# Kernel tuning notes

Hardware: AMD Instinct MI355X
Metric: run time of the kernel (lower is better)

The kernel has to match this reference:

```python
import jax, jax.numpy as jnp
import numpy as np

T, B, C = 4, 2, 128
LT, LH, LW = 8, 32, 32
NUM_HEADS = 8
HEAD_DIM = C // NUM_HEADS
THETA = 0.7
V_TH = 1.0
TAU = 2.0  # spikingjelly LIFNode default tau
N_WIN = (2, 2, 2)
TOPK = 4
EPS = 1e-5
ATAN_ALPHA = 2.0  # spikingjelly surrogate.ATan default


@jax.custom_vjp
def spike(x):
    return (x >= 0.0).astype(x.dtype)

def _spike_fwd(x):
    return spike(x), x

def _spike_bwd(x, g):
    s = (jnp.pi / 2.0) * ATAN_ALPHA * x
    return (g * (ATAN_ALPHA / 2.0) / (1.0 + s * s),)

spike.defvjp(_spike_fwd, _spike_bwd)


def lif(x_seq):
    """Multi-step LIF: v'=v+(x-v)/tau, spike at v>=V_TH, hard reset to 0 (detached)."""
    def step(v, x):
        v = v + (x - v) / TAU
        s = spike(v - V_TH)
        v = v * (1.0 - jax.lax.stop_gradient(s))  # detach_reset, v_reset=0
        return v, s
    _, s_seq = jax.lax.scan(step, jnp.zeros_like(x_seq[0]), x_seq)
    return s_seq


def bn(x, gamma, beta):
    # BatchNorm3d(track_running_stats=False) on [T*B, C, D, H, W]: batch stats per channel
    mean = x.mean(axis=(0, 1, 3, 4, 5), keepdims=True)
    var = x.var(axis=(0, 1, 3, 4, 5), keepdims=True)
    shp = (1, 1, -1, 1, 1, 1)
    return (x - mean) * jax.lax.rsqrt(var + EPS) * gamma.reshape(shp) + beta.reshape(shp)


def conv3d(x, w, pad):
    t, b = x.shape[:2]
    y = jax.lax.conv_general_dilated(
        x.reshape((t * b,) + x.shape[2:]), w,
        window_strides=(1, 1, 1), padding=[(pad, pad)] * 3,
        dimension_numbers=('NCDHW', 'OIDHW', 'NCDHW'))
    return y.reshape((t, b) + y.shape[1:])


def cdc_t(x, w):
    out = conv3d(x, w, 1)
    # central-difference temporal term: 1x1x1 conv with summed first/last temporal slices
    kd = w[:, :, 0].sum((-1, -2)) + w[:, :, 2].sum((-1, -2))  # [O, I]
    return out - THETA * jnp.einsum('oi,tbidhw->tbodhw', kd, x)


def to_wins(t):
    wt, wh, ww = N_WIN
    Tn, Bn, Cn, Lt, Lh, Lw = t.shape
    lt, lh, lw = Lt // wt, Lh // wh, Lw // ww
    t = t.reshape(Tn, Bn, Cn, wt, lt, wh, lh, ww, lw)
    t = t.transpose(0, 1, 3, 5, 7, 4, 6, 8, 2)
    return t.reshape(Tn, Bn, wt * wh * ww, lt * lh * lw, Cn)


def setup_inputs() -> dict:
    key = jax.random.key(0)
    ks = jax.random.split(key, 4)
    x = jax.random.normal(ks[0], (T, B, C, LT, LH, LW), jnp.float32)
    qw = jax.random.normal(ks[1], (C, C, 3, 3, 3), jnp.float32) / np.sqrt(C * 27)
    kw = jax.random.normal(ks[2], (C, C), jnp.float32) / np.sqrt(C)
    pw = jax.random.normal(ks[3], (C, C), jnp.float32) / np.sqrt(C)
    ones = jnp.ones((C,), jnp.float32)
    zeros = jnp.zeros((C,), jnp.float32)
    return {"x": x, "qw": qw, "q_gamma": ones, "q_beta": zeros,
            "kw": kw, "k_gamma": ones, "k_beta": zeros,
            "v_gamma": ones, "v_beta": zeros,
            "pw": pw, "p_gamma": ones, "p_beta": zeros}


def reference(x, qw, q_gamma, q_beta, kw, k_gamma, k_beta,
              v_gamma, v_beta, pw, p_gamma, p_beta):
    Tn, Bn, Cn, Lt, Lh, Lw = x.shape
    wt, wh, ww = N_WIN
    num_wins = wt * wh * ww
    lt, lh, lw = Lt // wt, Lh // wh, Lw // ww

    q_real = bn(cdc_t(x, qw), q_gamma, q_beta)
    k_real = bn(jnp.einsum('oi,tbidhw->tbodhw', kw, x), k_gamma, k_beta)

    # region-level routing from pre-spike activations
    q_region = to_wins(q_real).mean(axis=(0, 3))  # [B, W, C]
    k_region = to_wins(k_real).mean(axis=(0, 3))
    a_r = jnp.einsum('bwc,bvc->bwv', q_region, k_region) * (HEAD_DIM ** -0.5)
    k_eff = min(TOPK, num_wins)
    _, idx = jax.lax.top_k(a_r, k_eff)  # [B, W, k]

    q = lif(q_real)
    k = lif(k_real)
    v = lif(bn(x, v_gamma, v_beta))
    q_w = to_wins(q)  # [T,B,W,S,C]
    k_w = to_wins(k)
    v_w = to_wins(v)

    # gather routed windows per (batch, target window), mean-aggregate over top-k
    gather = jax.vmap(lambda src_b, idx_b: src_b[:, idx_b], in_axes=(1, 0), out_axes=1)
    k_agg = gather(k_w, idx).mean(axis=3)  # [T,B,W,S,C]
    v_agg = gather(v_w, idx).mean(axis=3)

    S = q_w.shape[3]
    q_h = q_w.reshape(Tn, Bn, num_wins, S, NUM_HEADS, HEAD_DIM)
    k_h = k_agg.reshape(Tn, Bn, num_wins, S, NUM_HEADS, HEAD_DIM)
    v_h = v_agg.reshape(Tn, Bn, num_wins, S, NUM_HEADS, HEAD_DIM)

    attn = (q_h * k_h).sum(axis=5, keepdims=True)  # [T,B,W,S,H,1]
    attn = lif(attn)
    out = (attn * v_h).reshape(Tn, Bn, num_wins, S, Cn)

    out = out.reshape(Tn, Bn, wt, wh, ww, lt, lh, lw, Cn)
    out = out.transpose(0, 1, 8, 2, 5, 3, 6, 4, 7).reshape(Tn, Bn, Cn, Lt, Lh, Lw)

    out = lif(out)
    out = bn(jnp.einsum('oi,tbidhw->tbodhw', pw, out), p_gamma, p_beta)
    return out
```

## Files before the change

kernel.cpp:

```cpp
#include <hip/hip_runtime.h>

#define TT 4
#define BB 2
#define CC 128
#define DD 8
#define HHH 32
#define WWW 32
#define PP (DD*HHH*WWW)
#define TSTRIDE (BB*CC*PP)
#define NWIN 8
#define SSS 1024
#define NHEAD 8
#define HDIM 16
#define THETA 0.7f
#define VTH 1.0f
#define NPERC (TT*BB*PP)
#define EPSf 1e-5f

typedef unsigned short ushortT;
typedef unsigned char ucharT;
typedef _Float16 half_t;
typedef _Float16 f16x8 __attribute__((ext_vector_type(8)));
typedef float    f32x16 __attribute__((ext_vector_type(16)));

typedef const __attribute__((address_space(1))) void* as1_cvp;
typedef __attribute__((address_space(3))) void* as3_vp;

__global__ __launch_bounds__(256) void prep_wmodT(const float* __restrict__ qw,
                                                  float* __restrict__ wmodT) {
    int oi = blockIdx.x*256 + threadIdx.x;
    if (oi >= CC*CC) return;
    int o  = oi >> 7;
    int ic = oi & 127;
    const float* wp = qw + (size_t)oi*27;
    float kd = 0.f;
    #pragma unroll
    for (int t=0; t<9; t++) kd += wp[t] + wp[18+t];
    #pragma unroll
    for (int t=0; t<27; t++) {
        float v = wp[t] - ((t==13) ? THETA*kd : 0.f);
        wmodT[((size_t)o*27 + t)*CC + ic] = v;
    }
}

__global__ __launch_bounds__(256) void prep_wfrag(const float* __restrict__ wmodT,
                                                  half_t* __restrict__ wfrag) {
    int id = blockIdx.x*256 + threadIdx.x;
    if (id >= 8*27*4*64) return;
    int lane = id & 63;
    int r = id >> 6;
    int m = r & 3; r >>= 2;
    int t = r % 27;
    int kb = r / 27;
    int o   = m*32 + (lane & 31);
    int ic0 = kb*16 + (lane>>5)*8;
    size_t base = ((size_t)(id>>6))*2*64*8 + (size_t)lane*8;
    #pragma unroll
    for (int j=0;j<8;j++){
        float v = wmodT[((size_t)o*27 + t)*CC + ic0 + j];
        half_t h = (half_t)v;
        half_t l = (half_t)(v - (float)h);
        wfrag[base + 0*64*8 + j] = h;
        wfrag[base + 1*64*8 + j] = l;
    }
}

__global__ __launch_bounds__(256) void prep_w1frag(const float* __restrict__ W,
                                                   half_t* __restrict__ frag) {
    int id = blockIdx.x*256 + threadIdx.x;
    if (id >= 2048) return;
    int lane = id & 63;
    int r = id >> 6;
    int m = r & 3;
    int kb = r >> 2;
    int o   = m*32 + (lane & 31);
    int ic0 = kb*16 + (lane>>5)*8;
    size_t base = ((size_t)(kb*4+m))*2*64*8 + (size_t)lane*8;
    #pragma unroll
    for (int j=0;j<8;j++){
        float v = W[(size_t)o*CC + ic0 + j];
        half_t h = (half_t)v;
        half_t l = (half_t)(v - (float)h);
        frag[base + 0*64*8 + j] = h;
        frag[base + 1*64*8 + j] = l;
    }
}

__global__ __launch_bounds__(256) void build_xsplit(const float* __restrict__ x,
                                                    half_t* __restrict__ xsp) {
    int id = blockIdx.x*256 + threadIdx.x;
    if (id >= 8*16*8*34*34) return;
    int wt = id % 34; int r = id/34;
    int hp = r % 34;  r /= 34;
    int dz = r % 8;   r /= 8;
    int icg = r & 15; int tb = r >> 4;
    bool inb = (hp>=1) & (hp<=32) & (wt>=1) & (wt<=32);
    half_t h8[8], l8[8];
    #pragma unroll
    for (int j=0;j<8;j++){
        float v = 0.f;
        if (inb)
            v = x[((size_t)(tb*CC + icg*8+j))*PP + (size_t)dz*1024 + (hp-1)*32 + (wt-1)];
        half_t h = (half_t)v;
        half_t l = (half_t)(v - (float)h);
        h8[j]=h; l8[j]=l;
    }
    #pragma unroll
    for (int sp=0; sp<2; sp++){
        size_t gu = (((((size_t)tb*2 + sp)*16 + icg)*8 + dz)*34 + hp)*34 + wt;
        half_t* dst = xsp + gu*8;
        const half_t* src = (sp==0)?h8:l8;
        #pragma unroll
        for (int j=0;j<8;j++) dst[j] = src[j];
    }
}

__global__ __launch_bounds__(512,2) void conv_mfma3(const half_t* __restrict__ xsp,
                                                    const half_t* __restrict__ wfrag,
                                                    float* __restrict__ y0,
                                                    float* __restrict__ y1) {
    extern __shared__ half_t slab[];
    int tid  = threadIdx.x;
    int wid  = tid >> 6;
    int lane = tid & 63;
    int ln   = lane & 31;
    int half_ = lane >> 5;
    int hg = blockIdx.x;
    int dp = blockIdx.y;
    int z  = blockIdx.z;
    int tb = z >> 1, kh = z & 1;
    int H0 = hg*4, d0 = dp*4;
    int r  = wid & 3;
    int q  = wid >> 2;
    float* y = kh ? y1 : y0;

    auto STAGE = [&](int bk, int bsel) {
        int kb = kh*4 + bk;
        half_t* bufp = slab + (size_t)bsel*(4896*8);
        #pragma unroll 1
        for (int k2=0; k2<10; k2++) {
            int u = tid + (k2<<9);
            if (u < 4896) {
                int sp  = (u >= 2448) ? 1 : 0;
                int r1  = u - sp*2448;
                int icg = (r1 >= 1224) ? 1 : 0;
                int p2  = r1 - icg*1224;
                int dzs = p2/204; int r3 = p2 - dzs*204;
                int hp  = r3/34;  int wt = r3 - hp*34;
                int dd  = d0 - 1 + dzs;
                const half_t* src = ((unsigned)dd < 8u)
                    ? &xsp[((((((size_t)tb*2 + sp)*16 + (kb*2+icg))*8 + dd)*34 + (H0+hp))*34 + wt)*8]
                    : &xsp[(size_t)ln*8];
                __builtin_amdgcn_global_load_lds((as1_cvp)src,
                    (as3_vp)(bufp + (size_t)u*8), 16, 0, 0);
            }
        }
    };

    f32x16 acc[2][4];
    #pragma unroll
    for (int dt=0;dt<2;dt++)
        #pragma unroll
        for (int m=0;m<4;m++)
            #pragma unroll
            for (int i=0;i<16;i++) acc[dt][m][i] = 0.f;

    f16x8 ca[4][2];
    #pragma unroll
    for (int m=0;m<4;m++)
        #pragma unroll
        for (int sp=0;sp<2;sp++)
            ca[m][sp] = *(const f16x8*)&wfrag[((((size_t)(kh*4*27)*4 + m)*2+sp)*64 + lane)*8];

    asm volatile("" ::: "memory");
    STAGE(0,0);
    STAGE(1,1);
    asm volatile("" ::: "memory");

    #pragma unroll 1
    for (int kk=0; kk<4; kk++) {
        int kb = kh*4 + kk;
        if (kk == 0) {
            if (wid < 5) asm volatile("s_waitcnt vmcnt(10)" ::: "memory");
            else         asm volatile("s_waitcnt vmcnt(9)"  ::: "memory");
        } else {
            asm volatile("s_waitcnt vmcnt(63)" ::: "memory");
        }
        __builtin_amdgcn_s_barrier();
        asm volatile("" ::: "memory");
        const half_t* bufp = slab + (size_t)(kk&1)*(4896*8);
        #pragma unroll 1
        for (int t=0; t<27; t++) {
            int dz=t/9; int rr=t-dz*9; int dh=rr/3; int dw=rr-dh*3;
            f16x8 cb[2][2];
            #pragma unroll
            for (int dt=0;dt<2;dt++){
                int unitb = (q*2 + dt + dz)*204 + (r+dh)*34 + (ln+dw);
                #pragma unroll
                for (int sp=0;sp<2;sp++)
                    cb[dt][sp] = *(const f16x8*)&bufp[(size_t)((sp*2+half_)*1224 + unitb)*8];
            }
            f16x8 na[4][2];
            int nt  = (t<26)? t+1 : 0;
            int nkb = (t<26)? kb  : ((kk<3)? kb+1 : kb);
            #pragma unroll
            for (int m=0;m<4;m++)
                #pragma unroll
                for (int sp=0;sp<2;sp++)
                    na[m][sp] = *(const f16x8*)&wfrag[((((size_t)(nkb*27+nt)*4+m)*2+sp)*64 + lane)*8];
            __builtin_amdgcn_s_setprio(1);
            #pragma unroll
            for (int dt=0;dt<2;dt++)
                #pragma unroll
                for (int m=0;m<4;m++) acc[dt][m] = __builtin_amdgcn_mfma_f32_32x32x16_f16(ca[m][0], cb[dt][0], acc[dt][m],0,0,0);
            #pragma unroll
            for (int dt=0;dt<2;dt++)
                #pragma unroll
                for (int m=0;m<4;m++) acc[dt][m] = __builtin_amdgcn_mfma_f32_32x32x16_f16(ca[m][0], cb[dt][1], acc[dt][m],0,0,0);
            #pragma unroll
            for (int dt=0;dt<2;dt++)
                #pragma unroll
                for (int m=0;m<4;m++) acc[dt][m] = __builtin_amdgcn_mfma_f32_32x32x16_f16(ca[m][1], cb[dt][0], acc[dt][m],0,0,0);
            __builtin_amdgcn_s_setprio(0);
            #pragma unroll
            for (int m=0;m<4;m++)
                #pragma unroll
                for (int sp=0;sp<2;sp++) ca[m][sp] = na[m][sp];
        }
        asm volatile("" ::: "memory");
        __builtin_amdgcn_s_barrier();
        asm volatile("" ::: "memory");
        if (kk < 2) STAGE(kk+2, kk&1);
    }

    int h = H0 + r;
    #pragma unroll
    for (int dt=0; dt<2; dt++) {
        int d = d0 + q*2 + dt;
        #pragma unroll
        for (int m=0; m<4; m++) {
            #pragma unroll
            for (int reg=0; reg<16; reg++) {
                int row = (reg&3) + 8*(reg>>2) + 4*half_;
                int o = m*32 + row;
                y[((size_t)tb*CC + o)*PP + d*1024 + h*32 + ln] = acc[dt][m][reg];
            }
        }
    }
}

__global__ __launch_bounds__(256) void conv_add(float* __restrict__ q,
                                                const float* __restrict__ p1) {
    size_t i = ((size_t)blockIdx.x*256 + threadIdx.x)*4;
    float4 a = *(const float4*)&q[i];
    float4 b = *(const float4*)&p1[i];
    a.x+=b.x; a.y+=b.y; a.z+=b.z; a.w+=b.w;
    *(float4*)&q[i] = a;
}

__global__ __launch_bounds__(256) void kgemm_mfma(const half_t* __restrict__ xsp,
                                                  const half_t* __restrict__ wk,
                                                  float* __restrict__ y) {
    int tid  = threadIdx.x;
    int wid  = tid >> 6;
    int lane = tid & 63;
    int ln   = lane & 31;
    int half_ = lane >> 5;
    int hg = blockIdx.x, d = blockIdx.y, tb = blockIdx.z;
    int h = hg*4 + wid;

    f32x16 acc[4];
    #pragma unroll
    for (int m=0;m<4;m++)
        #pragma unroll
        for (int i=0;i<16;i++) acc[m][i] = 0.f;

    #pragma unroll 2
    for (int kb=0; kb<8; kb++) {
        f16x8 b[2];
        #pragma unroll
        for (int sp=0; sp<2; sp++) {
            size_t gu = (((((size_t)tb*2 + sp)*16 + (kb*2+half_))*8 + d)*34 + (h+1))*34 + (ln+1);
            b[sp] = *(const f16x8*)&xsp[gu*8];
        }
        #pragma unroll
        for (int m=0; m<4; m++) {
            const half_t* wb = wk + ((size_t)(kb*4+m))*2*64*8 + (size_t)lane*8;
            f16x8 a0 = *(const f16x8*)&wb[0*64*8];
            f16x8 a1 = *(const f16x8*)&wb[1*64*8];
            acc[m] = __builtin_amdgcn_mfma_f32_32x32x16_f16(a0, b[0], acc[m],0,0,0);
            acc[m] = __builtin_amdgcn_mfma_f32_32x32x16_f16(a0, b[1], acc[m],0,0,0);
            acc[m] = __builtin_amdgcn_mfma_f32_32x32x16_f16(a1, b[0], acc[m],0,0,0);
        }
    }
    #pragma unroll
    for (int m=0; m<4; m++) {
        #pragma unroll
        for (int reg=0; reg<16; reg++) {
            int row = (reg&3) + 8*(reg>>2) + 4*half_;
            int o = m*32 + row;
            y[((size_t)tb*CC + o)*PP + d*1024 + h*32 + ln] = acc[m][reg];
        }
    }
}

__global__ __launch_bounds__(256) void pgemm_mfma(const ushortT* __restrict__ spkb,
                                                  const half_t* __restrict__ wp,
                                                  float* __restrict__ y) {
    int tid  = threadIdx.x;
    int wid  = tid >> 6;
    int lane = tid & 63;
    int ln   = lane & 31;
    int half_ = lane >> 5;
    int hg = blockIdx.x, d = blockIdx.y, tb = blockIdx.z;
    int h = hg*4 + wid;
    int p = d*1024 + h*32 + ln;

    f32x16 acc[4];
    #pragma unroll
    for (int m=0;m<4;m++)
        #pragma unroll
        for (int i=0;i<16;i++) acc[m][i] = 0.f;

    #pragma unroll 2
    for (int kb=0; kb<8; kb++) {
        f16x8 b = *(const f16x8*)&spkb[(((size_t)tb*16 + (kb*2+half_))*PP + p)*8];
        #pragma unroll
        for (int m=0; m<4; m++) {
            const half_t* wb = wp + ((size_t)(kb*4+m))*2*64*8 + (size_t)lane*8;
            f16x8 a0 = *(const f16x8*)&wb[0*64*8];
            f16x8 a1 = *(const f16x8*)&wb[1*64*8];
            acc[m] = __builtin_amdgcn_mfma_f32_32x32x16_f16(a0, b, acc[m],0,0,0);
            acc[m] = __builtin_amdgcn_mfma_f32_32x32x16_f16(a1, b, acc[m],0,0,0);
        }
    }
    #pragma unroll
    for (int m=0; m<4; m++) {
        #pragma unroll
        for (int reg=0; reg<16; reg++) {
            int row = (reg&3) + 8*(reg>>2) + 4*half_;
            int o = m*32 + row;
            y[((size_t)tb*CC + o)*PP + p] = acc[m][reg];
        }
    }
}

__global__ __launch_bounds__(128) void win_stats(const float* __restrict__ q,
        const float* __restrict__ k, const float* __restrict__ x,
        float* __restrict__ rsum, float* __restrict__ rsq) {
    int blk = blockIdx.x;
    int src = blk >> 11;
    int r   = blk & 2047;
    const float* base = (src==0) ? q : ((src==1) ? k : x);
    int c  = r & 127;
    int wi = (r >> 7) & 7;
    int b  = r >> 10;
    int wd = wi>>2, wh = (wi>>1)&1, ww = wi&1;
    int tid = threadIdx.x;
    float s=0.f, s2=0.f;
    for (int t=0;t<TT;t++){
        const float* p = base + ((size_t)(t*BB+b)*CC + c)*PP;
        for (int si=tid; si<SSS; si+=128){
            int ld = si>>8, lh=(si>>4)&15, lw=si&15;
            float v = p[((wd*4+ld)<<10) + ((wh*16+lh)<<5) + (ww*16+lw)];
            s += v; s2 += v*v;
        }
    }
    __shared__ float ls[128], ls2[128];
    ls[tid]=s; ls2[tid]=s2; __syncthreads();
    for (int off=64;off>0;off>>=1){
        if(tid<off){ ls[tid]+=ls[tid+off]; ls2[tid]+=ls2[tid+off]; }
        __syncthreads();
    }
    if (tid==0){ rsum[blk]=ls[0]; rsq[blk]=ls2[0]; }
}

__global__ __launch_bounds__(384) void stats_fin(const float* __restrict__ rsum,
        const float* __restrict__ rsq, float* __restrict__ sums) {
    int tid = threadIdx.x;
    int src = tid >> 7, c = tid & 127;
    float s=0.f, s2=0.f;
    for (int bw=0; bw<16; bw++){
        int idx = src*2048 + bw*128 + c;
        s  += rsum[idx];
        s2 += rsq[idx];
    }
    sums[src*256 + c]       = s;
    sums[src*256 + 128 + c] = s2;
}

__global__ __launch_bounds__(128) void route_topk(const float* __restrict__ qreg,
        const float* __restrict__ kreg,
        const float* __restrict__ qsum, const float* __restrict__ qsq,
        const float* __restrict__ ksum, const float* __restrict__ ksq,
        const float* __restrict__ qg, const float* __restrict__ qb,
        const float* __restrict__ kg, const float* __restrict__ kb,
        int* __restrict__ idxout) {
    __shared__ float qn[16*128], kn[16*128], ar[16*8];
    int tid = threadIdx.x;
    for (int e=tid; e<16*128; e+=128){
        int c = e&127;
        float qm = qsum[c]*(1.f/NPERC);
        float qv = qsq[c]*(1.f/NPERC) - qm*qm;
        float qr = rsqrtf(qv + EPSf);
        qn[e] = (qreg[e]*(1.f/(TT*SSS)) - qm)*qr*qg[c] + qb[c];
        float km = ksum[c]*(1.f/NPERC);
        float kv = ksq[c]*(1.f/NPERC) - km*km;
        float kr = rsqrtf(kv + EPSf);
        kn[e] = (kreg[e]*(1.f/(TT*SSS)) - km)*kr*kg[c] + kb[c];
    }
    __syncthreads();
    {
        int b = tid>>6, w=(tid>>3)&7, v=tid&7;
        float s=0.f;
        for (int c=0;c<128;c++) s += qn[(b*8+w)*128+c]*kn[(b*8+v)*128+c];
        ar[(b*8+w)*8+v] = s * 0.25f;
    }
    __syncthreads();
    if (tid < 16){
        const float* row = &ar[tid*8];
        bool used[8] = {false,false,false,false,false,false,false,false};
        for (int j=0;j<4;j++){
            int best=0; float bv=-3.0e38f;
            for (int v=0; v<8; v++){
                if (!used[v] && row[v] > bv){ bv=row[v]; best=v; }
            }
            used[best]=true;
            idxout[tid*4+j]=best;
        }
    }
}

__global__ __launch_bounds__(256) void lif_bn_win3(const float* __restrict__ qin,
        const float* __restrict__ kin, const float* __restrict__ xin,
        ucharT* __restrict__ qs, ucharT* __restrict__ ks, ucharT* __restrict__ vs,
        const float* __restrict__ stats,
        const float* __restrict__ qg, const float* __restrict__ qb,
        const float* __restrict__ kg, const float* __restrict__ kb,
        const float* __restrict__ vg, const float* __restrict__ vb) {
    int src = blockIdx.y;
    const float* in  = (src==0) ? qin : ((src==1) ? kin : xin);
    ucharT*      spk = (src==0) ? qs  : ((src==1) ? ks  : vs);
    const float* gamma = (src==0) ? qg : ((src==1) ? kg : vg);
    const float* beta  = (src==0) ? qb : ((src==1) ? kb : vb);
    int e = blockIdx.x*256 + threadIdx.x;
    if (e >= BB*CC*PP) return;
    int p = e & (PP-1);
    int c = (e >> 13) & 127;
    int b = e >> 20;
    float mean = stats[src*256 + c]*(1.f/NPERC);
    float var  = stats[src*256 + 128 + c]*(1.f/NPERC) - mean*mean;
    float sc = rsqrtf(var+EPSf)*gamma[c];
    float sh = beta[c] - mean*sc;
    int d = p>>10, h=(p>>5)&31, w=p&31;
    int wi = ((d>>2)*2 + (h>>4))*2 + (w>>4);
    int si = (((d&3)<<4) + (h&15))*16 + (w&15);
    size_t widx = ((size_t)(b*NWIN+wi)*CC + c)*SSS + si;
    float v=0.f;
    #pragma unroll
    for (int t=0;t<TT;t++){
        float xn = in[(size_t)t*TSTRIDE + e]*sc + sh;
        v = (v+xn)*0.5f;
        float s = (v>=VTH)?1.f:0.f;
        spk[(size_t)t*TSTRIDE + widx] = (ucharT)(v>=VTH ? 1 : 0);
        v *= (1.f - s);
    }
}

__global__ __launch_bounds__(256) void attn_lif(const ucharT* __restrict__ qspk,
        const ucharT* __restrict__ kspk, const ucharT* __restrict__ vspk,
        const int* __restrict__ idx, ushortT* __restrict__ spkb) {
    int id = blockIdx.x*256 + threadIdx.x;
    if (id >= BB*NWIN*NHEAD*SSS) return;
    int s  = id & 1023;
    int hh = (id>>10) & 7;
    int wi = (id>>13) & 7;
    int b  = id>>16;
    int bw = b*NWIN+wi;
    size_t qbase = ((size_t)bw*CC + hh*HDIM)*SSS + s;
    size_t sbase[4];
    #pragma unroll
    for (int j=0;j<4;j++){
        int src = idx[bw*4+j];
        sbase[j] = ((size_t)(b*NWIN+src)*CC + hh*HDIM)*SSS + s;
    }
    int wd = wi>>2, wh = (wi>>1)&1, ww = wi&1;
    int d3 = wd*4 + (s>>8), h3 = wh*16 + ((s>>4)&15), w3 = ww*16 + (s&15);
    int p  = (d3<<10) + (h3<<5) + w3;

    float v=0.f;
    float v2[16];
    #pragma unroll
    for (int dd=0; dd<16; dd++) v2[dd]=0.f;

    #pragma unroll 1
    for (int t=0;t<TT;t++){
        size_t toff = (size_t)t*TSTRIDE;
        int km[16], vm[16];
        #pragma unroll
        for (int dd=0;dd<16;dd++){ km[dd]=0; vm[dd]=0; }
        #pragma unroll
        for (int j=0;j<4;j++){
            const ucharT* kp = kspk+toff+sbase[j];
            const ucharT* vp = vspk+toff+sbase[j];
            #pragma unroll
            for (int dd=0; dd<16; dd++){
                km[dd] += kp[(size_t)dd*SSS];
                vm[dd] += vp[(size_t)dd*SSS];
            }
        }
        const ucharT* qp = qspk+toff+qbase;
        int atti=0;
        #pragma unroll
        for (int dd=0;dd<16;dd++) atti += (int)qp[(size_t)dd*SSS]*km[dd];
        float att = (float)atti * 0.25f;
        v = (v+att)*0.5f;
        float sp = (v>=VTH)?1.f:0.f;
        v *= (1.f-sp);
        float spq = sp*0.25f;
        union { ushortT u[8]; uint4 q4; } pk0, pk1;
        #pragma unroll
        for (int dd=0;dd<16;dd++){
            float ov = spq*(float)vm[dd];
            v2[dd] = (v2[dd]+ov)*0.5f;
            float s2 = (v2[dd]>=VTH)?1.f:0.f;
            v2[dd] *= (1.f-s2);
            ushortT bs = (s2 != 0.f) ? (ushortT)0x3C00 : (ushortT)0;
            if (dd < 8) pk0.u[dd] = bs; else pk1.u[dd-8] = bs;
        }
        int tb2 = t*BB + b;
        size_t base = (((size_t)tb2*16 + hh*2)*PP + p)*8;
        *(uint4*)&spkb[base] = pk0.q4;
        *(uint4*)&spkb[base + (size_t)PP*8] = pk1.q4;
    }
}

__global__ __launch_bounds__(256) void pstats_part(const float* __restrict__ xin,
        float* __restrict__ part_sum, float* __restrict__ part_sq) {
    int blk = blockIdx.x;
    int c = blk & 127, tb = blk >> 7;
    int tid = threadIdx.x;
    const float* p = xin + ((size_t)tb*CC + c)*PP;
    float s=0.f, s2=0.f;
    for (int i=tid; i<PP; i+=256){ float v=p[i]; s+=v; s2+=v*v; }
    __shared__ float ls[256], ls2[256];
    ls[tid]=s; ls2[tid]=s2; __syncthreads();
    for (int off=128; off>0; off>>=1){
        if (tid<off){ ls[tid]+=ls[tid+off]; ls2[tid]+=ls2[tid+off]; }
        __syncthreads();
    }
    if (tid==0){ part_sum[blk]=ls[0]; part_sq[blk]=ls2[0]; }
}

__global__ __launch_bounds__(128) void pstats_fin(const float* __restrict__ part_sum,
        const float* __restrict__ part_sq, float* __restrict__ sum,
        float* __restrict__ sq) {
    int c = threadIdx.x;
    float s=0.f, s2=0.f;
    for (int tb=0; tb<8; tb++){
        s  += part_sum[tb*128+c];
        s2 += part_sq[tb*128+c];
    }
    sum[c]=s; sq[c]=s2;
}

__global__ __launch_bounds__(256) void bn_apply(const float* __restrict__ xin,
        float* __restrict__ yout,
        const float* __restrict__ sum, const float* __restrict__ sq,
        const float* __restrict__ gamma, const float* __restrict__ beta) {
    size_t i = (size_t)blockIdx.x*256 + threadIdx.x;
    if (i >= (size_t)TT*BB*CC*PP) return;
    int c = (int)((i>>13)&127);
    float mean = sum[c]*(1.f/NPERC);
    float var  = sq[c]*(1.f/NPERC) - mean*mean;
    float sc = rsqrtf(var+EPSf)*gamma[c];
    float sh = beta[c] - mean*sc;
    yout[i] = xin[i]*sc + sh;
}

extern "C" void kernel_launch(void* const* d_in, const int* in_sizes, int n_in,
                              void* d_out, int out_size, void* d_ws, size_t ws_size,
                              hipStream_t stream) {
    const float* x  = (const float*)d_in[0];
    const float* qw = (const float*)d_in[1];
    const float* qg = (const float*)d_in[2];
    const float* qb = (const float*)d_in[3];
    const float* kw = (const float*)d_in[4];
    const float* kg = (const float*)d_in[5];
    const float* kb = (const float*)d_in[6];
    const float* vg = (const float*)d_in[7];
    const float* vb = (const float*)d_in[8];
    const float* pw = (const float*)d_in[9];
    const float* pg = (const float*)d_in[10];
    const float* pb = (const float*)d_in[11];
    float* out = (float*)d_out;
    float* ws  = (float*)d_ws;

    const size_t NEL = (size_t)TT*TSTRIDE;
    float* qconv = ws;
    float* kconv = ws + NEL;
    float* qspk  = ws + 2*NEL;
    float* kspk  = ws + 3*NEL;
    float* vspk  = ws + 4*NEL;
    float* wmodT = ws + 5*NEL;
    float* stats = ws + 5*NEL + 442368;
    float *qsum=stats,     *qsq=stats+128,  *ksum=stats+256, *ksq=stats+384,
          *psum=stats+768, *psq=stats+896;
    float* rsum = stats + 1024;
    float* rsq  = rsum + 6144;
    float* ppart_sum = rsq + 6144;
    float* ppart_sq  = ppart_sum + 1024;
    int*   idxp = (int*)(ppart_sq + 1024);

    half_t* xsp    = (half_t*)(ws + 2*NEL);
    half_t* wfrag  = (half_t*)(ws + 4*NEL);
    half_t* wkfrag = (half_t*)(ws + 4*NEL) + 884736;
    half_t* wpfrag = (half_t*)(ws + 4*NEL);
    ushortT* spkb  = (ushortT*)(ws + NEL);
    float*   pconv = ws + 2*NEL;
    float*   part1 = kconv;

    prep_wmodT<<<64,256,0,stream>>>(qw, wmodT);
    prep_wfrag<<<216,256,0,stream>>>(wmodT, wfrag);
    prep_w1frag<<<8,256,0,stream>>>(kw, wkfrag);
    build_xsplit<<<4624,256,0,stream>>>(x, xsp);
    {
        static bool attr_set = false;
        const int shmem = 2*4896*8*(int)sizeof(half_t);
        if (!attr_set) {
            hipFuncSetAttribute((const void*)conv_mfma3,
                                hipFuncAttributeMaxDynamicSharedMemorySize, shmem);
            attr_set = true;
        }
        dim3 cg(8,2,16);
        conv_mfma3<<<cg,512,shmem,stream>>>(xsp, wfrag, qconv, part1);
    }
    conv_add<<<8192,256,0,stream>>>(qconv, part1);
    {
        dim3 gg(8,8,8);
        kgemm_mfma<<<gg,256,0,stream>>>(xsp, wkfrag, kconv);
    }
    win_stats<<<6144,128,0,stream>>>(qconv, kconv, x, rsum, rsq);
    stats_fin<<<1,384,0,stream>>>(rsum, rsq, stats);
    route_topk<<<1,128,0,stream>>>(rsum, rsum+2048, qsum,qsq,ksum,ksq,qg,qb,kg,kb,idxp);
    {
        dim3 lg(8192,3);
        lif_bn_win3<<<lg,256,0,stream>>>(qconv,kconv,x,
                                         (ucharT*)qspk,(ucharT*)kspk,(ucharT*)vspk,
                                         stats, qg,qb,kg,kb,vg,vb);
    }
    attn_lif<<<512,256,0,stream>>>((const ucharT*)qspk,(const ucharT*)kspk,
                                   (const ucharT*)vspk,idxp,spkb);
    prep_w1frag<<<8,256,0,stream>>>(pw, wpfrag);
    {
        dim3 gg(8,8,8);
        pgemm_mfma<<<gg,256,0,stream>>>(spkb, wpfrag, pconv);
    }
    pstats_part<<<1024,256,0,stream>>>(pconv, ppart_sum, ppart_sq);
    pstats_fin<<<1,128,0,stream>>>(ppart_sum, ppart_sq, psum, psq);
    bn_apply<<<32768,256,0,stream>>>(pconv, out, psum, psq, pg, pb);
}
```

Baseline: 419.7 us.

## Fuse conv partial-sum add into consumers and merge small reduction kernels

Drops the conv_add pass: the two conv partial outputs are summed on the fly inside win_stats and lif_bn_win3. stats_fin is merged into route_topk, and pstats_fin is folded into bn_apply, which now re-reduces the partials per thread. The workspace layout is reshuffled so both partial buffers stay live, and the setprio hints around the MFMA block are removed. This saves one full read-modify-write pass and two tiny launches, at the cost of an extra read wherever the q tensor is consumed and redundant partial-sum reads in bn_apply.

Result: faster. 396.8 us (-5.5%).

```diff
diff --git a/kernel.cpp b/kernel.cpp
--- a/kernel.cpp
+++ b/kernel.cpp
@@ -208,7 +208,6 @@
                 #pragma unroll
                 for (int sp=0;sp<2;sp++)
                     na[m][sp] = *(const f16x8*)&wfrag[((((size_t)(nkb*27+nt)*4+m)*2+sp)*64 + lane)*8];
-            __builtin_amdgcn_s_setprio(1);
             #pragma unroll
             for (int dt=0;dt<2;dt++)
                 #pragma unroll
@@ -221,7 +220,6 @@
             for (int dt=0;dt<2;dt++)
                 #pragma unroll
                 for (int m=0;m<4;m++) acc[dt][m] = __builtin_amdgcn_mfma_f32_32x32x16_f16(ca[m][1], cb[dt][0], acc[dt][m],0,0,0);
-            __builtin_amdgcn_s_setprio(0);
             #pragma unroll
             for (int m=0;m<4;m++)
                 #pragma unroll
@@ -247,15 +245,6 @@
             }
         }
     }
-}
-
-__global__ __launch_bounds__(256) void conv_add(float* __restrict__ q,
-                                                const float* __restrict__ p1) {
-    size_t i = ((size_t)blockIdx.x*256 + threadIdx.x)*4;
-    float4 a = *(const float4*)&q[i];
-    float4 b = *(const float4*)&p1[i];
-    a.x+=b.x; a.y+=b.y; a.z+=b.z; a.w+=b.w;
-    *(float4*)&q[i] = a;
 }
 
 __global__ __launch_bounds__(256) void kgemm_mfma(const half_t* __restrict__ xsp,
@@ -345,13 +334,14 @@
     }
 }
 
-__global__ __launch_bounds__(128) void win_stats(const float* __restrict__ q,
+__global__ __launch_bounds__(128) void win_stats(const float* __restrict__ q0,
+        const float* __restrict__ q1,
         const float* __restrict__ k, const float* __restrict__ x,
         float* __restrict__ rsum, float* __restrict__ rsq) {
     int blk = blockIdx.x;
     int src = blk >> 11;
     int r   = blk & 2047;
-    const float* base = (src==0) ? q : ((src==1) ? k : x);
+    const float* base = (src==0) ? q0 : ((src==1) ? k : x);
     int c  = r & 127;
     int wi = (r >> 7) & 7;
     int b  = r >> 10;
@@ -359,10 +349,14 @@
     int tid = threadIdx.x;
     float s=0.f, s2=0.f;
     for (int t=0;t<TT;t++){
-        const float* p = base + ((size_t)(t*BB+b)*CC + c)*PP;
+        size_t off0 = ((size_t)(t*BB+b)*CC + c)*PP;
+        const float* p  = base + off0;
+        const float* p2 = q1 + off0;
         for (int si=tid; si<SSS; si+=128){
             int ld = si>>8, lh=(si>>4)&15, lw=si&15;
-            float v = p[((wd*4+ld)<<10) + ((wh*16+lh)<<5) + (ww*16+lw)];
+            int o = ((wd*4+ld)<<10) + ((wh*16+lh)<<5) + (ww*16+lw);
+            float v = p[o];
+            if (src==0) v += p2[o];
             s += v; s2 += v*v;
         }
     }
@@ -375,42 +369,40 @@
     if (tid==0){ rsum[blk]=ls[0]; rsq[blk]=ls2[0]; }
 }
 
-__global__ __launch_bounds__(384) void stats_fin(const float* __restrict__ rsum,
-        const float* __restrict__ rsq, float* __restrict__ sums) {
-    int tid = threadIdx.x;
-    int src = tid >> 7, c = tid & 127;
-    float s=0.f, s2=0.f;
-    for (int bw=0; bw<16; bw++){
-        int idx = src*2048 + bw*128 + c;
-        s  += rsum[idx];
-        s2 += rsq[idx];
-    }
-    sums[src*256 + c]       = s;
-    sums[src*256 + 128 + c] = s2;
-}
-
-__global__ __launch_bounds__(128) void route_topk(const float* __restrict__ qreg,
-        const float* __restrict__ kreg,
-        const float* __restrict__ qsum, const float* __restrict__ qsq,
-        const float* __restrict__ ksum, const float* __restrict__ ksq,
+__global__ __launch_bounds__(384) void route_fin(const float* __restrict__ rsum,
+        const float* __restrict__ rsq,
         const float* __restrict__ qg, const float* __restrict__ qb,
         const float* __restrict__ kg, const float* __restrict__ kb,
-        int* __restrict__ idxout) {
+        float* __restrict__ stats, int* __restrict__ idxout) {
     __shared__ float qn[16*128], kn[16*128], ar[16*8];
+    __shared__ float csum[384], csq[384];
     int tid = threadIdx.x;
-    for (int e=tid; e<16*128; e+=128){
+    {
+        int src = tid >> 7, c = tid & 127;
+        float s=0.f, s2=0.f;
+        for (int bw=0; bw<16; bw++){
+            int idx = src*2048 + bw*128 + c;
+            s  += rsum[idx];
+            s2 += rsq[idx];
+        }
+        stats[src*256 + c]       = s;
+        stats[src*256 + 128 + c] = s2;
+        csum[tid]=s; csq[tid]=s2;
+    }
+    __syncthreads();
+    for (int e=tid; e<16*128; e+=384){
         int c = e&127;
-        float qm = qsum[c]*(1.f/NPERC);
-        float qv = qsq[c]*(1.f/NPERC) - qm*qm;
+        float qm = csum[c]*(1.f/NPERC);
+        float qv = csq[c]*(1.f/NPERC) - qm*qm;
         float qr = rsqrtf(qv + EPSf);
-        qn[e] = (qreg[e]*(1.f/(TT*SSS)) - qm)*qr*qg[c] + qb[c];
-        float km = ksum[c]*(1.f/NPERC);
-        float kv = ksq[c]*(1.f/NPERC) - km*km;
+        qn[e] = (rsum[e]*(1.f/(TT*SSS)) - qm)*qr*qg[c] + qb[c];
+        float km = csum[128+c]*(1.f/NPERC);
+        float kv = csq[128+c]*(1.f/NPERC) - km*km;
         float kr = rsqrtf(kv + EPSf);
-        kn[e] = (kreg[e]*(1.f/(TT*SSS)) - km)*kr*kg[c] + kb[c];
+        kn[e] = (rsum[2048+e]*(1.f/(TT*SSS)) - km)*kr*kg[c] + kb[c];
     }
     __syncthreads();
-    {
+    if (tid < 128){
         int b = tid>>6, w=(tid>>3)&7, v=tid&7;
         float s=0.f;
         for (int c=0;c<128;c++) s += qn[(b*8+w)*128+c]*kn[(b*8+v)*128+c];
@@ -431,7 +423,8 @@
     }
 }
 
-__global__ __launch_bounds__(256) void lif_bn_win3(const float* __restrict__ qin,
+__global__ __launch_bounds__(256) void lif_bn_win3(const float* __restrict__ q0,
+        const float* __restrict__ q1,
         const float* __restrict__ kin, const float* __restrict__ xin,
         ucharT* __restrict__ qs, ucharT* __restrict__ ks, ucharT* __restrict__ vs,
         const float* __restrict__ stats,
@@ -439,7 +432,7 @@
         const float* __restrict__ kg, const float* __restrict__ kb,
         const float* __restrict__ vg, const float* __restrict__ vb) {
     int src = blockIdx.y;
-    const float* in  = (src==0) ? qin : ((src==1) ? kin : xin);
+    const float* in  = (src==0) ? q0 : ((src==1) ? kin : xin);
     ucharT*      spk = (src==0) ? qs  : ((src==1) ? ks  : vs);
     const float* gamma = (src==0) ? qg : ((src==1) ? kg : vg);
     const float* beta  = (src==0) ? qb : ((src==1) ? kb : vb);
@@ -459,7 +452,10 @@
     float v=0.f;
     #pragma unroll
     for (int t=0;t<TT;t++){
-        float xn = in[(size_t)t*TSTRIDE + e]*sc + sh;
+        size_t ti = (size_t)t*TSTRIDE + e;
+        float raw = in[ti];
+        if (src==0) raw += q1[ti];
+        float xn = raw*sc + sh;
         v = (v+xn)*0.5f;
         float s = (v>=VTH)?1.f:0.f;
         spk[(size_t)t*TSTRIDE + widx] = (ucharT)(v>=VTH ? 1 : 0);
@@ -552,27 +548,21 @@
     if (tid==0){ part_sum[blk]=ls[0]; part_sq[blk]=ls2[0]; }
 }
 
-__global__ __launch_bounds__(128) void pstats_fin(const float* __restrict__ part_sum,
-        const float* __restrict__ part_sq, float* __restrict__ sum,
-        float* __restrict__ sq) {
-    int c = threadIdx.x;
-    float s=0.f, s2=0.f;
-    for (int tb=0; tb<8; tb++){
-        s  += part_sum[tb*128+c];
-        s2 += part_sq[tb*128+c];
-    }
-    sum[c]=s; sq[c]=s2;
-}
-
 __global__ __launch_bounds__(256) void bn_apply(const float* __restrict__ xin,
         float* __restrict__ yout,
-        const float* __restrict__ sum, const float* __restrict__ sq,
+        const float* __restrict__ part_sum, const float* __restrict__ part_sq,
         const float* __restrict__ gamma, const float* __restrict__ beta) {
     size_t i = (size_t)blockIdx.x*256 + threadIdx.x;
     if (i >= (size_t)TT*BB*CC*PP) return;
     int c = (int)((i>>13)&127);
-    float mean = sum[c]*(1.f/NPERC);
-    float var  = sq[c]*(1.f/NPERC) - mean*mean;
+    float s=0.f, s2=0.f;
+    #pragma unroll
+    for (int tb=0; tb<8; tb++){
+        s  += part_sum[tb*128+c];
+        s2 += part_sq[tb*128+c];
+    }
+    float mean = s*(1.f/NPERC);
+    float var  = s2*(1.f/NPERC) - mean*mean;
     float sc = rsqrtf(var+EPSf)*gamma[c];
     float sh = beta[c] - mean*sc;
     yout[i] = xin[i]*sc + sh;
@@ -597,28 +587,28 @@
     float* ws  = (float*)d_ws;
 
     const size_t NEL = (size_t)TT*TSTRIDE;
-    float* qconv = ws;
-    float* kconv = ws + NEL;
-    float* qspk  = ws + 2*NEL;
-    float* kspk  = ws + 3*NEL;
-    float* vspk  = ws + 4*NEL;
-    float* wmodT = ws + 5*NEL;
-    float* stats = ws + 5*NEL + 442368;
-    float *qsum=stats,     *qsq=stats+128,  *ksum=stats+256, *ksq=stats+384,
-          *psum=stats+768, *psq=stats+896;
+    float* part0 = ws;
+    float* part1 = ws + NEL;
+    half_t* xsp  = (half_t*)(ws + 2*NEL);
+    const size_t KCONV_OFF = 2*NEL + 10747904;
+    float* kconv = ws + KCONV_OFF;
+    float* wf_base = ws + KCONV_OFF + NEL;
+    half_t* wfrag  = (half_t*)wf_base;
+    half_t* wkfrag = (half_t*)(wf_base + 442368);
+    float*  wmodT  = wf_base + 442368 + 16384;
+    float* stats = ws + 5*NEL;
     float* rsum = stats + 1024;
     float* rsq  = rsum + 6144;
     float* ppart_sum = rsq + 6144;
     float* ppart_sq  = ppart_sum + 1024;
     int*   idxp = (int*)(ppart_sq + 1024);
 
-    half_t* xsp    = (half_t*)(ws + 2*NEL);
-    half_t* wfrag  = (half_t*)(ws + 4*NEL);
-    half_t* wkfrag = (half_t*)(ws + 4*NEL) + 884736;
-    half_t* wpfrag = (half_t*)(ws + 4*NEL);
-    ushortT* spkb  = (ushortT*)(ws + NEL);
-    float*   pconv = ws + 2*NEL;
-    float*   part1 = kconv;
+    ucharT* qspk = (ucharT*)(ws + 2*NEL);
+    ucharT* kspk = (ucharT*)(ws + 2*NEL) + 8388608;
+    ucharT* vspk = (ucharT*)(ws + 2*NEL) + 16777216;
+    ushortT* spkb  = (ushortT*)ws;
+    half_t* wpfrag = (half_t*)(ws + NEL);
+    float*  pconv  = ws + KCONV_OFF;
 
     prep_wmodT<<<64,256,0,stream>>>(qw, wmodT);
     prep_wfrag<<<216,256,0,stream>>>(wmodT, wfrag);
@@ -633,30 +623,26 @@
             attr_set = true;
         }
         dim3 cg(8,2,16);
-        conv_mfma3<<<cg,512,shmem,stream>>>(xsp, wfrag, qconv, part1);
-    }
-    conv_add<<<8192,256,0,stream>>>(qconv, part1);
+        conv_mfma3<<<cg,512,shmem,stream>>>(xsp, wfrag, part0, part1);
+    }
     {
         dim3 gg(8,8,8);
         kgemm_mfma<<<gg,256,0,stream>>>(xsp, wkfrag, kconv);
     }
-    win_stats<<<6144,128,0,stream>>>(qconv, kconv, x, rsum, rsq);
-    stats_fin<<<1,384,0,stream>>>(rsum, rsq, stats);
-    route_topk<<<1,128,0,stream>>>(rsum, rsum+2048, qsum,qsq,ksum,ksq,qg,qb,kg,kb,idxp);
+    win_stats<<<6144,128,0,stream>>>(part0, part1, kconv, x, rsum, rsq);
+    route_fin<<<1,384,0,stream>>>(rsum, rsq, qg,qb,kg,kb, stats, idxp);
     {
         dim3 lg(8192,3);
-        lif_bn_win3<<<lg,256,0,stream>>>(qconv,kconv,x,
-                                         (ucharT*)qspk,(ucharT*)kspk,(ucharT*)vspk,
+        lif_bn_win3<<<lg,256,0,stream>>>(part0,part1,kconv,x,
+                                         qspk,kspk,vspk,
                                          stats, qg,qb,kg,kb,vg,vb);
     }
-    attn_lif<<<512,256,0,stream>>>((const ucharT*)qspk,(const ucharT*)kspk,
-                                   (const ucharT*)vspk,idxp,spkb);
+    attn_lif<<<512,256,0,stream>>>(qspk,kspk,vspk,idxp,spkb);
     prep_w1frag<<<8,256,0,stream>>>(pw, wpfrag);
     {
         dim3 gg(8,8,8);
         pgemm_mfma<<<gg,256,0,stream>>>(spkb, wpfrag, pconv);
     }
     pstats_part<<<1024,256,0,stream>>>(pconv, ppart_sum, ppart_sq);
-    pstats_fin<<<1,128,0,stream>>>(ppart_sum, ppart_sq, psum, psq);
-    bn_apply<<<32768,256,0,stream>>>(pconv, out, psum, psq, pg, pb);
-}
+    bn_apply<<<32768,256,0,stream>>>(pconv, out, ppart_sum, ppart_sq, pg, pb);
+}
```
